# Kernel tuning notes

Measured on AMD Instinct MI355X. Metric: run time of the kernel, lower is better.

Reference implementation:

```python
import jax, jax.numpy as jnp
import numpy as np

DIM = 2048
MAX_LEN = 8192
EPS = 1e-6


def rms_norm(x, w):
    # x / sqrt(mean(x^2) + eps) * w
    rms = jnp.sqrt(jnp.mean(x * x, axis=-1, keepdims=True) + EPS)
    return x / rms * w


def setup_inputs() -> dict:
    key = jax.random.key(0)
    ks = jax.random.split(key, 12)
    s = 0.02  # weight init scale
    return {
        "x": jax.random.normal(ks[0], (1, DIM), jnp.float32),
        "cacheK": jax.random.normal(ks[1], (MAX_LEN, DIM), jnp.float32),
        "cacheV": jax.random.normal(ks[2], (MAX_LEN, DIM), jnp.float32),
        "attn_norm_w": jnp.ones((DIM,), jnp.float32),
        "q_w": jax.random.normal(ks[3], (DIM, DIM), jnp.float32) * s,
        "q_b": jnp.zeros((DIM,), jnp.float32),
        "k_w": jax.random.normal(ks[4], (DIM, DIM), jnp.float32) * s,
        "k_b": jnp.zeros((DIM,), jnp.float32),
        "v_w": jax.random.normal(ks[5], (DIM, DIM), jnp.float32) * s,
        "v_b": jnp.zeros((DIM,), jnp.float32),
        "o_w": jax.random.normal(ks[6], (DIM, DIM), jnp.float32) * s,
        "o_b": jnp.zeros((DIM,), jnp.float32),
        "mlp_norm_w": jnp.ones((DIM,), jnp.float32),
        "fc1_w": jax.random.normal(ks[7], (4 * DIM, DIM), jnp.float32) * s,
        "fc1_b": jnp.zeros((4 * DIM,), jnp.float32),
        "fc2_w": jax.random.normal(ks[8], (DIM, 4 * DIM), jnp.float32) * s,
        "fc2_b": jnp.zeros((DIM,), jnp.float32),
        "pos": 4096,
    }


def reference(x, cacheK, cacheV, attn_norm_w, q_w, q_b, k_w, k_b, v_w, v_b,
              o_w, o_b, mlp_norm_w, fc1_w, fc1_b, fc2_w, fc2_b, pos):
    dim = x.shape[-1]
    xn = rms_norm(x, attn_norm_w)                     # [1, d]
    q = xn @ q_w.T + q_b                              # [1, d]
    k = xn @ k_w.T + k_b
    v = xn @ v_w.T + v_b
    cacheK = cacheK.at[pos].set(k[0])                 # scatter write new KV
    cacheV = cacheV.at[pos].set(v[0])
    # attention over cache[:pos+1] (pos is a static Python int)
    scores = (cacheK[:pos + 1] @ q[0]) / np.sqrt(dim)  # [pos+1]
    probs = jax.nn.softmax(scores, axis=0)
    attn = (probs @ cacheV[:pos + 1])[None, :]        # [1, d]
    x = x + attn @ o_w.T + o_b
    hn = rms_norm(x, mlp_norm_w)
    h = jax.nn.gelu(hn @ fc1_w.T + fc1_b, approximate=False)  # exact erf GELU
    x = x + h @ fc2_w.T + fc2_b
    return x
```

## Files before the change

### kernel.cpp

```cpp
#include <hip/hip_runtime.h>

#define DIMN 2048
#define HDIM 8192

#define WS_Q    2048
#define WS_ATTN 4096
#define WS_X1   6144
#define WS_H    10240
#define WS_SC   18432

__device__ __forceinline__ float dot4(float4 w, float4 a) {
    return w.x * a.x + w.y * a.y + w.z * a.z + w.w * a.w;
}

__device__ __forceinline__ float waveSum(float v) {
#pragma unroll
    for (int off = 32; off > 0; off >>= 1) v += __shfl_down(v, off, 64);
    return v;
}

__device__ __forceinline__ float blockSum256(float v, float* red) {
    v = waveSum(v);
    int wave = threadIdx.x >> 6, lane = threadIdx.x & 63;
    if (lane == 0) red[wave] = v;
    __syncthreads();
    float r = red[0] + red[1] + red[2] + red[3];
    __syncthreads();
    return r;
}

__device__ __forceinline__ float blockMax256(float v, float* red) {
#pragma unroll
    for (int off = 32; off > 0; off >>= 1) v = fmaxf(v, __shfl_down(v, off, 64));
    int wave = threadIdx.x >> 6, lane = threadIdx.x & 63;
    if (lane == 0) red[wave] = v;
    __syncthreads();
    float r = fmaxf(fmaxf(red[0], red[1]), fmaxf(red[2], red[3]));
    __syncthreads();
    return r;
}

__global__ __launch_bounds__(256) void k_qkv(
        const float* __restrict__ x, const float* __restrict__ anw,
        float* __restrict__ ws,
        const float* __restrict__ qw, const float* __restrict__ qb,
        const float* __restrict__ kw, const float* __restrict__ kb,
        const float* __restrict__ vw, const float* __restrict__ vb,
        float* __restrict__ cacheK, float* __restrict__ cacheV,
        const int* __restrict__ posp) {
    __shared__ float xn[DIMN];
    __shared__ float red[4];
    int tid = threadIdx.x, wave = tid >> 6, lane = tid & 63;
    int row = blockIdx.x * 4 + wave;
    int mat = row >> 11, r = row & (DIMN - 1);
    const float* W = (mat == 0) ? qw : (mat == 1) ? kw : vw;
    const float* B = (mat == 0) ? qb : (mat == 1) ? kb : vb;
    const float4* wrow = reinterpret_cast<const float4*>(W + (size_t)r * DIMN);
    float4 wr[8];
#pragma unroll
    for (int i = 0; i < 8; ++i) wr[i] = wrow[lane + i * 64];
    float4 a = reinterpret_cast<const float4*>(x)[tid * 2];
    float4 b = reinterpret_cast<const float4*>(x)[tid * 2 + 1];
    float ss = dot4(a, a) + dot4(b, b);
    ss = blockSum256(ss, red);
    float scale = rsqrtf(ss / (float)DIMN + 1e-6f);
    float4 wa = reinterpret_cast<const float4*>(anw)[tid * 2];
    float4 wb = reinterpret_cast<const float4*>(anw)[tid * 2 + 1];
    reinterpret_cast<float4*>(xn)[tid * 2] =
        make_float4(a.x * scale * wa.x, a.y * scale * wa.y, a.z * scale * wa.z, a.w * scale * wa.w);
    reinterpret_cast<float4*>(xn)[tid * 2 + 1] =
        make_float4(b.x * scale * wb.x, b.y * scale * wb.y, b.z * scale * wb.z, b.w * scale * wb.w);
    if (blockIdx.x == 0) {
        float4 z = make_float4(0.f, 0.f, 0.f, 0.f);
        reinterpret_cast<float4*>(ws + WS_ATTN)[tid * 2] = z;
        reinterpret_cast<float4*>(ws + WS_ATTN)[tid * 2 + 1] = z;
    }
    __syncthreads();
    const float4* xv = reinterpret_cast<const float4*>(xn);
    float acc = 0.f;
#pragma unroll
    for (int i = 0; i < 8; ++i) acc += dot4(wr[i], xv[lane + i * 64]);
    acc = waveSum(acc);
    if (lane == 0) {
        float y = acc + B[r];
        if (mat == 0) {
            ws[WS_Q + r] = y;
        } else {
            float* dst = (mat == 1) ? cacheK : cacheV;
            dst[(size_t)posp[0] * DIMN + r] = y;
        }
    }
}

__global__ __launch_bounds__(256) void k_scores(
        const float* __restrict__ cacheK, float* __restrict__ ws,
        const int* __restrict__ posp) {
    int wave = threadIdx.x >> 6, lane = threadIdx.x & 63;
    int t = blockIdx.x * 4 + wave;
    int L = posp[0] + 1;
    if (t >= L) return;
    const float4* krow = reinterpret_cast<const float4*>(cacheK + (size_t)t * DIMN);
    const float4* qv = reinterpret_cast<const float4*>(ws + WS_Q);
    float acc = 0.f;
#pragma unroll
    for (int i = 0; i < 8; ++i) {
        int ch = lane + i * 64;
        acc += dot4(krow[ch], qv[ch]);
    }
    acc = waveSum(acc);
    if (lane == 0) ws[WS_SC + t] = acc * 0.022097086912079608f;
}

__global__ __launch_bounds__(256) void k_av(
        const float* __restrict__ cacheV, float* __restrict__ ws,
        const int* __restrict__ posp) {
    __shared__ float red[4];
    int tid = threadIdx.x;
    int L = posp[0] + 1;
    float m = -1e30f;
    for (int i = tid; i < L; i += 256) m = fmaxf(m, ws[WS_SC + i]);
    m = blockMax256(m, red);
    float s = 0.f;
    for (int i = tid; i < L; i += 256) s += expf(ws[WS_SC + i] - m);
    s = blockSum256(s, red);
    float inv = 1.0f / s;
    int T = gridDim.y, chunk = blockIdx.y;
    int t0 = (int)((long long)chunk * L / T);
    int t1 = (int)((long long)(chunk + 1) * L / T);
    int c2 = blockIdx.x * 256 + tid;
    const float2* Vp = reinterpret_cast<const float2*>(cacheV);
    float a0 = 0.f, a1 = 0.f;
    for (int t = t0; t < t1; ++t) {
        float p = expf(ws[WS_SC + t] - m) * inv;
        float2 v = Vp[(size_t)t * (DIMN / 2) + c2];
        a0 += p * v.x;
        a1 += p * v.y;
    }
    atomicAdd(&ws[WS_ATTN + 2 * c2], a0);
    atomicAdd(&ws[WS_ATTN + 2 * c2 + 1], a1);
}

__global__ __launch_bounds__(256) void k_oproj(
        const float* __restrict__ x, const float* __restrict__ ow,
        const float* __restrict__ ob, float* __restrict__ ws) {
    int wave = threadIdx.x >> 6, lane = threadIdx.x & 63;
    int r = blockIdx.x * 4 + wave;
    const float4* wrow = reinterpret_cast<const float4*>(ow + (size_t)r * DIMN);
    const float4* av = reinterpret_cast<const float4*>(ws + WS_ATTN);
    float acc = 0.f;
#pragma unroll
    for (int i = 0; i < 8; ++i) {
        int ch = lane + i * 64;
        acc += dot4(wrow[ch], av[ch]);
    }
    acc = waveSum(acc);
    if (lane == 0) ws[WS_X1 + r] = x[r] + acc + ob[r];
}

__global__ __launch_bounds__(256) void k_fc1(
        const float* __restrict__ w1, const float* __restrict__ b1,
        const float* __restrict__ mnw, float* __restrict__ ws) {
    __shared__ float hn[DIMN];
    __shared__ float red[4];
    int tid = threadIdx.x, wave = tid >> 6, lane = tid & 63;
    int r = blockIdx.x * 4 + wave;
    const float4* wrow = reinterpret_cast<const float4*>(w1 + (size_t)r * DIMN);
    float4 wr[8];
#pragma unroll
    for (int i = 0; i < 8; ++i) wr[i] = wrow[lane + i * 64];
    float4 a = reinterpret_cast<const float4*>(ws + WS_X1)[tid * 2];
    float4 b = reinterpret_cast<const float4*>(ws + WS_X1)[tid * 2 + 1];
    float ss = dot4(a, a) + dot4(b, b);
    ss = blockSum256(ss, red);
    float scale = rsqrtf(ss / (float)DIMN + 1e-6f);
    float4 wa = reinterpret_cast<const float4*>(mnw)[tid * 2];
    float4 wb = reinterpret_cast<const float4*>(mnw)[tid * 2 + 1];
    reinterpret_cast<float4*>(hn)[tid * 2] =
        make_float4(a.x * scale * wa.x, a.y * scale * wa.y, a.z * scale * wa.z, a.w * scale * wa.w);
    reinterpret_cast<float4*>(hn)[tid * 2 + 1] =
        make_float4(b.x * scale * wb.x, b.y * scale * wb.y, b.z * scale * wb.z, b.w * scale * wb.w);
    __syncthreads();
    const float4* hv = reinterpret_cast<const float4*>(hn);
    float acc = 0.f;
#pragma unroll
    for (int i = 0; i < 8; ++i) acc += dot4(wr[i], hv[lane + i * 64]);
    acc = waveSum(acc);
    if (lane == 0) {
        float t = acc + b1[r];
        ws[WS_H + r] = 0.5f * t * (1.0f + erff(t * 0.70710678118654752f));
    }
}

__global__ __launch_bounds__(256) void k_fc2(
        const float* __restrict__ w2, const float* __restrict__ b2,
        const float* __restrict__ ws, float* __restrict__ out) {
    int wave = threadIdx.x >> 6, lane = threadIdx.x & 63;
    int r = blockIdx.x * 4 + wave;
    const float4* wrow = reinterpret_cast<const float4*>(w2 + (size_t)r * HDIM);
    const float4* hv = reinterpret_cast<const float4*>(ws + WS_H);
    float acc = 0.f;
#pragma unroll
    for (int i = 0; i < 32; ++i) {
        int ch = lane + i * 64;
        acc += dot4(wrow[ch], hv[ch]);
    }
    acc = waveSum(acc);
    if (lane == 0) out[r] = ws[WS_X1 + r] + acc + b2[r];
}

extern "C" void kernel_launch(void* const* d_in, const int* in_sizes, int n_in,
                              void* d_out, int out_size, void* d_ws, size_t ws_size,
                              hipStream_t stream) {
    const float* x   = (const float*)d_in[0];
    float* cacheK    = (float*)d_in[1];
    float* cacheV    = (float*)d_in[2];
    const float* anw = (const float*)d_in[3];
    const float* qw  = (const float*)d_in[4];
    const float* qb  = (const float*)d_in[5];
    const float* kw  = (const float*)d_in[6];
    const float* kb  = (const float*)d_in[7];
    const float* vw  = (const float*)d_in[8];
    const float* vb  = (const float*)d_in[9];
    const float* ow  = (const float*)d_in[10];
    const float* ob  = (const float*)d_in[11];
    const float* mnw = (const float*)d_in[12];
    const float* w1  = (const float*)d_in[13];
    const float* b1  = (const float*)d_in[14];
    const float* w2  = (const float*)d_in[15];
    const float* b2  = (const float*)d_in[16];
    const int* posp  = (const int*)d_in[17];
    float* ws = (float*)d_ws;
    float* out = (float*)d_out;

    k_qkv<<<1536, 256, 0, stream>>>(x, anw, ws, qw, qb, kw, kb, vw, vb, cacheK, cacheV, posp);
    k_scores<<<1025, 256, 0, stream>>>(cacheK, ws, posp);
    k_av<<<dim3(4, 128), 256, 0, stream>>>(cacheV, ws, posp);
    k_oproj<<<512, 256, 0, stream>>>(x, ow, ob, ws);
    k_fc1<<<2048, 256, 0, stream>>>(w1, b1, mnw, ws);
    k_fc2<<<512, 256, 0, stream>>>(w2, b2, ws, out);
}
```

Before: 332.5 us.

## Fuse decoder step into single cooperative persistent kernel with grid syncs

```diff
diff --git a/kernel.cpp b/kernel.cpp
--- a/kernel.cpp
+++ b/kernel.cpp
@@ -1,4 +1,7 @@
 #include <hip/hip_runtime.h>
+#include <hip/hip_cooperative_groups.h>
+
+namespace cg = cooperative_groups;
 
 #define DIMN 2048
 #define HDIM 8192
@@ -38,6 +41,182 @@
     float r = fmaxf(fmaxf(red[0], red[1]), fmaxf(red[2], red[3]));
     __syncthreads();
     return r;
+}
+
+__device__ __forceinline__ void gsync(cg::grid_group& g) {
+    __threadfence();
+    g.sync();
+    __threadfence();
+}
+
+__global__ __launch_bounds__(256, 2) void k_fused(
+        const float* __restrict__ x,
+        float* __restrict__ cacheK, float* __restrict__ cacheV,
+        const float* __restrict__ anw,
+        const float* __restrict__ qw, const float* __restrict__ qb,
+        const float* __restrict__ kw, const float* __restrict__ kb,
+        const float* __restrict__ vw, const float* __restrict__ vb,
+        const float* __restrict__ ow, const float* __restrict__ ob,
+        const float* __restrict__ mnw,
+        const float* __restrict__ w1, const float* __restrict__ b1,
+        const float* __restrict__ w2, const float* __restrict__ b2,
+        const int* __restrict__ posp,
+        float* __restrict__ ws, float* __restrict__ out) {
+    cg::grid_group grid = cg::this_grid();
+    __shared__ float xn[DIMN];
+    __shared__ float red[4];
+    const int tid = threadIdx.x, wave = tid >> 6, lane = tid & 63;
+    const int bid = blockIdx.x;
+    const int gw = bid * 4 + wave;
+    const int pos = posp[0];
+    const int L = pos + 1;
+
+    {
+        float4 a = reinterpret_cast<const float4*>(x)[tid * 2];
+        float4 b = reinterpret_cast<const float4*>(x)[tid * 2 + 1];
+        float ss = blockSum256(dot4(a, a) + dot4(b, b), red);
+        float scale = rsqrtf(ss / (float)DIMN + 1e-6f);
+        float4 wa = reinterpret_cast<const float4*>(anw)[tid * 2];
+        float4 wb = reinterpret_cast<const float4*>(anw)[tid * 2 + 1];
+        reinterpret_cast<float4*>(xn)[tid * 2] =
+            make_float4(a.x * scale * wa.x, a.y * scale * wa.y,
+                        a.z * scale * wa.z, a.w * scale * wa.w);
+        reinterpret_cast<float4*>(xn)[tid * 2 + 1] =
+            make_float4(b.x * scale * wb.x, b.y * scale * wb.y,
+                        b.z * scale * wb.z, b.w * scale * wb.w);
+        if (bid == 0) {
+            float4 z = make_float4(0.f, 0.f, 0.f, 0.f);
+            reinterpret_cast<float4*>(ws + WS_ATTN)[tid * 2] = z;
+            reinterpret_cast<float4*>(ws + WS_ATTN)[tid * 2 + 1] = z;
+        }
+        __syncthreads();
+        const float4* xv = reinterpret_cast<const float4*>(xn);
+        for (int row = gw; row < 3 * DIMN; row += 2048) {
+            int mat = row >> 11, r = row & (DIMN - 1);
+            const float* W = (mat == 0) ? qw : (mat == 1) ? kw : vw;
+            const float* B = (mat == 0) ? qb : (mat == 1) ? kb : vb;
+            const float4* wrow = reinterpret_cast<const float4*>(W + (size_t)r * DIMN);
+            float acc = 0.f;
+#pragma unroll
+            for (int i = 0; i < 8; ++i) {
+                int ch = lane + i * 64;
+                acc += dot4(wrow[ch], xv[ch]);
+            }
+            acc = waveSum(acc);
+            if (lane == 0) {
+                float y = acc + B[r];
+                if (mat == 0) {
+                    ws[WS_Q + r] = y;
+                } else {
+                    float* dst = (mat == 1) ? cacheK : cacheV;
+                    dst[(size_t)pos * DIMN + r] = y;
+                }
+            }
+        }
+    }
+    gsync(grid);
+
+    {
+        const float4* qv = reinterpret_cast<const float4*>(ws + WS_Q);
+        for (int t = gw; t < L; t += 2048) {
+            const float4* krow = reinterpret_cast<const float4*>(cacheK + (size_t)t * DIMN);
+            float acc = 0.f;
+#pragma unroll
+            for (int i = 0; i < 8; ++i) {
+                int ch = lane + i * 64;
+                acc += dot4(krow[ch], qv[ch]);
+            }
+            acc = waveSum(acc);
+            if (lane == 0) ws[WS_SC + t] = acc * 0.022097086912079608f;
+        }
+    }
+    gsync(grid);
+
+    {
+        float m = -1e30f;
+        for (int i = tid; i < L; i += 256) m = fmaxf(m, ws[WS_SC + i]);
+        m = blockMax256(m, red);
+        float s = 0.f;
+        for (int i = tid; i < L; i += 256) s += expf(ws[WS_SC + i] - m);
+        s = blockSum256(s, red);
+        float inv = 1.0f / s;
+        int chunk = bid >> 2;
+        int t0 = (int)((long long)chunk * L / 128);
+        int t1 = (int)((long long)(chunk + 1) * L / 128);
+        int c2 = (bid & 3) * 256 + tid;
+        const float2* Vp = reinterpret_cast<const float2*>(cacheV);
+        float a0 = 0.f, a1 = 0.f;
+        for (int t = t0; t < t1; ++t) {
+            float p = expf(ws[WS_SC + t] - m) * inv;
+            float2 v = Vp[(size_t)t * (DIMN / 2) + c2];
+            a0 += p * v.x;
+            a1 += p * v.y;
+        }
+        atomicAdd(&ws[WS_ATTN + 2 * c2], a0);
+        atomicAdd(&ws[WS_ATTN + 2 * c2 + 1], a1);
+    }
+    gsync(grid);
+
+    {
+        int r = gw;
+        const float4* wrow = reinterpret_cast<const float4*>(ow + (size_t)r * DIMN);
+        const float4* av = reinterpret_cast<const float4*>(ws + WS_ATTN);
+        float acc = 0.f;
+#pragma unroll
+        for (int i = 0; i < 8; ++i) {
+            int ch = lane + i * 64;
+            acc += dot4(wrow[ch], av[ch]);
+        }
+        acc = waveSum(acc);
+        if (lane == 0) ws[WS_X1 + r] = x[r] + acc + ob[r];
+    }
+    gsync(grid);
+
+    {
+        float4 a = reinterpret_cast<const float4*>(ws + WS_X1)[tid * 2];
+        float4 b = reinterpret_cast<const float4*>(ws + WS_X1)[tid * 2 + 1];
+        float ss = blockSum256(dot4(a, a) + dot4(b, b), red);
+        float scale = rsqrtf(ss / (float)DIMN + 1e-6f);
+        float4 wa = reinterpret_cast<const float4*>(mnw)[tid * 2];
+        float4 wb = reinterpret_cast<const float4*>(mnw)[tid * 2 + 1];
+        reinterpret_cast<float4*>(xn)[tid * 2] =
+            make_float4(a.x * scale * wa.x, a.y * scale * wa.y,
+                        a.z * scale * wa.z, a.w * scale * wa.w);
+        reinterpret_cast<float4*>(xn)[tid * 2 + 1] =
+            make_float4(b.x * scale * wb.x, b.y * scale * wb.y,
+                        b.z * scale * wb.z, b.w * scale * wb.w);
+        __syncthreads();
+        const float4* hv = reinterpret_cast<const float4*>(xn);
+        for (int row = gw; row < HDIM; row += 2048) {
+            const float4* wrow = reinterpret_cast<const float4*>(w1 + (size_t)row * DIMN);
+            float acc = 0.f;
+#pragma unroll
+            for (int i = 0; i < 8; ++i) {
+                int ch = lane + i * 64;
+                acc += dot4(wrow[ch], hv[ch]);
+            }
+            acc = waveSum(acc);
+            if (lane == 0) {
+                float t = acc + b1[row];
+                ws[WS_H + row] = 0.5f * t * (1.0f + erff(t * 0.70710678118654752f));
+            }
+        }
+    }
+    gsync(grid);
+
+    {
+        const float4* hv = reinterpret_cast<const float4*>(ws + WS_H);
+        int r = gw;
+        const float4* wrow = reinterpret_cast<const float4*>(w2 + (size_t)r * HDIM);
+        float acc = 0.f;
+#pragma unroll
+        for (int i = 0; i < 32; ++i) {
+            int ch = lane + i * 64;
+            acc += dot4(wrow[ch], hv[ch]);
+        }
+        acc = waveSum(acc);
+        if (lane == 0) out[r] = ws[WS_X1 + r] + acc + b2[r];
+    }
 }
 
 __global__ __launch_bounds__(256) void k_qkv(
@@ -61,8 +240,7 @@
     for (int i = 0; i < 8; ++i) wr[i] = wrow[lane + i * 64];
     float4 a = reinterpret_cast<const float4*>(x)[tid * 2];
     float4 b = reinterpret_cast<const float4*>(x)[tid * 2 + 1];
-    float ss = dot4(a, a) + dot4(b, b);
-    ss = blockSum256(ss, red);
+    float ss = blockSum256(dot4(a, a) + dot4(b, b), red);
     float scale = rsqrtf(ss / (float)DIMN + 1e-6f);
     float4 wa = reinterpret_cast<const float4*>(anw)[tid * 2];
     float4 wb = reinterpret_cast<const float4*>(anw)[tid * 2 + 1];
@@ -83,9 +261,8 @@
     acc = waveSum(acc);
     if (lane == 0) {
         float y = acc + B[r];
-        if (mat == 0) {
-            ws[WS_Q + r] = y;
-        } else {
+        if (mat == 0) ws[WS_Q + r] = y;
+        else {
             float* dst = (mat == 1) ? cacheK : cacheV;
             dst[(size_t)posp[0] * DIMN + r] = y;
         }
@@ -170,8 +347,7 @@
     for (int i = 0; i < 8; ++i) wr[i] = wrow[lane + i * 64];
     float4 a = reinterpret_cast<const float4*>(ws + WS_X1)[tid * 2];
     float4 b = reinterpret_cast<const float4*>(ws + WS_X1)[tid * 2 + 1];
-    float ss = dot4(a, a) + dot4(b, b);
-    ss = blockSum256(ss, red);
+    float ss = blockSum256(dot4(a, a) + dot4(b, b), red);
     float scale = rsqrtf(ss / (float)DIMN + 1e-6f);
     float4 wa = reinterpret_cast<const float4*>(mnw)[tid * 2];
     float4 wb = reinterpret_cast<const float4*>(mnw)[tid * 2 + 1];
@@ -232,10 +408,17 @@
     float* ws = (float*)d_ws;
     float* out = (float*)d_out;
 
-    k_qkv<<<1536, 256, 0, stream>>>(x, anw, ws, qw, qb, kw, kb, vw, vb, cacheK, cacheV, posp);
-    k_scores<<<1025, 256, 0, stream>>>(cacheK, ws, posp);
-    k_av<<<dim3(4, 128), 256, 0, stream>>>(cacheV, ws, posp);
-    k_oproj<<<512, 256, 0, stream>>>(x, ow, ob, ws);
-    k_fc1<<<2048, 256, 0, stream>>>(w1, b1, mnw, ws);
-    k_fc2<<<512, 256, 0, stream>>>(w2, b2, ws, out);
-}
+    void* args[] = {&x, &cacheK, &cacheV, &anw, &qw, &qb, &kw, &kb, &vw, &vb,
+                    &ow, &ob, &mnw, &w1, &b1, &w2, &b2, &posp, &ws, &out};
+    hipError_t e = hipLaunchCooperativeKernel((void*)k_fused, dim3(512), dim3(256),
+                                              args, 0, stream);
+    if (e != hipSuccess) {
+        (void)hipGetLastError();
+        k_qkv<<<1536, 256, 0, stream>>>(x, anw, ws, qw, qb, kw, kb, vw, vb, cacheK, cacheV, posp);
+        k_scores<<<1025, 256, 0, stream>>>(cacheK, ws, posp);
+        k_av<<<dim3(4, 128), 256, 0, stream>>>(cacheV, ws, posp);
+        k_oproj<<<512, 256, 0, stream>>>(x, ow, ob, ws);
+        k_fc1<<<2048, 256, 0, stream>>>(w1, b1, mnw, ws);
+        k_fc2<<<512, 256, 0, stream>>>(w2, b2, ws, out);
+    }
+}
```

Measured after the change: 1.107 ms. 233% more time.
